# Optimization experiments

Hardware: AMD Instinct MI355X
Metric: run time of the kernel (lower is better)

The kernel has to match this reference:

```python
import jax, jax.numpy as jnp
import numpy as np

B, C, T, H = 2, 1024, 2048, 16
D = C // H  # head dim = 64
SCALE = 1.0 / np.sqrt(D)
NEG_INF = jnp.float32(-1e30)


def setup_inputs() -> dict:
    key = jax.random.key(0)
    ks = jax.random.split(key, 10)
    x = jax.random.normal(ks[0], (B, C, T), dtype=jnp.float32)
    mask = jax.random.randint(ks[1], (B, 1, T), 0, 2).astype(bool)
    mask = mask.at[:, :, 0].set(True)  # avoid all-masked rows -> NaN softmax
    w = 1.0 / np.sqrt(C)
    Wq = jax.random.normal(ks[2], (C, C), dtype=jnp.float32) * w
    bq = jax.random.normal(ks[3], (C,), dtype=jnp.float32) * 0.01
    Wk = jax.random.normal(ks[4], (C, C), dtype=jnp.float32) * w
    bk = jax.random.normal(ks[5], (C,), dtype=jnp.float32) * 0.01
    Wv = jax.random.normal(ks[6], (C, C), dtype=jnp.float32) * w
    bv = jax.random.normal(ks[7], (C,), dtype=jnp.float32) * 0.01
    Wp = jax.random.normal(ks[8], (C, C), dtype=jnp.float32) * w
    bp = jax.random.normal(ks[9], (C,), dtype=jnp.float32) * 0.01
    return {"x": x, "mask": mask, "Wq": Wq, "bq": bq, "Wk": Wk, "bk": bk,
            "Wv": Wv, "bv": bv, "Wp": Wp, "bp": bp}


def _proj(W, b, x):
    # Conv1d with kernel_size=1: per-timestep linear on [B, C, T]
    return jnp.einsum('oc,bct->bot', W, x) + b[:, None]


def _heads(y):
    # [B, C, T] -> [B, H, T, D]
    return y.reshape(B, H, D, T).transpose(0, 1, 3, 2)


def reference(x, mask, Wq, bq, Wk, bk, Wv, bv, Wp, bp):
    q = _heads(_proj(Wq, bq, x))  # [B,H,T,D]
    k = _heads(_proj(Wk, bk, x))
    v = _heads(_proj(Wv, bv, x))
    att = jnp.einsum('bhqd,bhkd->bhqk', q * SCALE, k)  # [B,H,T,T]
    att = jnp.where(mask[:, :, None, :], att, NEG_INF)  # mask keys
    att = jax.nn.softmax(att, axis=-1)
    vm = v * mask[:, :, :, None].astype(v.dtype)  # zero masked values
    out = jnp.einsum('bhqk,bhkd->bhqd', att, vm)  # [B,H,T,D]
    out = out.transpose(0, 1, 3, 2).reshape(B, C, T)
    out = _proj(Wp, bp, out) * mask.astype(x.dtype)  # [B,C,T]
    return (out, mask)
```

## Files before the change

### kernel.cpp

```cpp
#include <hip/hip_runtime.h>
#include <hip/hip_bf16.h>
#include <math.h>

#define BB 2
#define CC 1024
#define TT 2048
#define HH 16
#define DD 64

using short8   = __attribute__((ext_vector_type(8))) short;
using floatx4  = __attribute__((ext_vector_type(4))) float;
using floatx16 = __attribute__((ext_vector_type(16))) float;
typedef unsigned short ushort_t;

#define MFMA(a, b, c) __builtin_amdgcn_mfma_f32_16x16x32_bf16((a), (b), (c), 0, 0, 0)
#define MFMA32(a, b, c) __builtin_amdgcn_mfma_f32_32x32x16_bf16((a), (b), (c), 0, 0, 0)

#define QSC 0.18033688011112042f

#define PMAGIC   8404857.0f
#define PZERO_BF 0.97265625f

__device__ __forceinline__ ushort_t f2bf(float f) {
    unsigned int u = __float_as_uint(f);
    u += 0x7FFFu + ((u >> 16) & 1u);
    return (ushort_t)(u >> 16);
}
__device__ __forceinline__ float bf2f(ushort_t h) {
    return __uint_as_float(((unsigned int)h) << 16);
}
__device__ __forceinline__ ushort_t f2bf_t(float f) {
    return (ushort_t)(__float_as_uint(f) >> 16);
}
__device__ __forceinline__ unsigned int packtrunc(float a, float b) {
    return __builtin_amdgcn_perm(__float_as_uint(b), __float_as_uint(a),
                                 0x07060302u);
}
__device__ __forceinline__ unsigned int pack2bf_exp(float s0, float s1) {
    float f0 = fmaf(s0, 128.0f, PMAGIC);
    float f1 = fmaf(s1, 128.0f, PMAGIC);
    return __builtin_amdgcn_perm(__float_as_uint(f1), __float_as_uint(f0),
                                 0x05040100u);
}
__device__ __forceinline__ void load_lds16(const void* g, void* s) {
    __builtin_amdgcn_global_load_lds(
        (const __attribute__((address_space(1))) void*)g,
        (__attribute__((address_space(3))) void*)s, 16, 0, 0);
}

static constexpr size_t B0       = 65536;
static constexpr size_t XT_OFF   = B0;
static constexpr size_t WQKV_OFF = XT_OFF   + 8388608;
static constexpr size_t WP_OFF   = WQKV_OFF + 6291456;
static constexpr size_t Q_OFF    = WP_OFF   + 2097152;
static constexpr size_t K_OFF    = Q_OFF    + 8388608;
static constexpr size_t V_OFF    = K_OFF    + 8388608;
static constexpr size_t OP_OFF   = V_OFF    + 8388608;
static constexpr size_t ML_OFF   = OP_OFF   + 16777216;

__global__ __launch_bounds__(256) void prep_kernel(
    const float* __restrict__ x, const float* __restrict__ Wq,
    const float* __restrict__ Wk, const float* __restrict__ Wv,
    const float* __restrict__ Wp, const unsigned int* __restrict__ mraw,
    ushort_t* __restrict__ XT, ushort_t* __restrict__ WQKV,
    ushort_t* __restrict__ WP, float* __restrict__ maskf,
    int* __restrict__ nmcnt, float* __restrict__ out_tail) {
    __shared__ float tile[64][65];
    const int bid = blockIdx.x;
    const int tid = threadIdx.x;
    if (bid < 4096) {
        const int idx = bid * 256 + tid;
        if (idx < 786432) {
            int row = idx >> 8;
            int qc  = idx & 255;
            const float* src = row < 1024 ? Wq : (row < 2048 ? Wk : Wv);
            float4 v = *(const float4*)&src[(size_t)(row & 1023) * CC + qc * 4];
            ushort4 pk; pk.x = f2bf(v.x); pk.y = f2bf(v.y);
            pk.z = f2bf(v.z); pk.w = f2bf(v.w);
            *(ushort4*)&WQKV[(size_t)idx * 4] = pk;
        } else {
            int j = idx - 786432;
            float4 v = *(const float4*)&Wp[(size_t)j * 4];
            ushort4 pk; pk.x = f2bf(v.x); pk.y = f2bf(v.y);
            pk.z = f2bf(v.z); pk.w = f2bf(v.w);
            *(ushort4*)&WP[(size_t)j * 4] = pk;
        }
    } else if (bid < 5120) {
        const int xb = bid - 4096;
        const int t0 = (xb & 31) * 64, c0 = ((xb >> 5) & 15) * 64, b = xb >> 9;
        const int tc = tid & 15, tr = tid >> 4;
        #pragma unroll
        for (int p = 0; p < 4; p++) {
            int cl = tr + p * 16;
            float4 v = *(const float4*)&x[((size_t)b * CC + c0 + cl) * TT + t0 + tc * 4];
            tile[cl][tc * 4 + 0] = v.x; tile[cl][tc * 4 + 1] = v.y;
            tile[cl][tc * 4 + 2] = v.z; tile[cl][tc * 4 + 3] = v.w;
        }
        __syncthreads();
        #pragma unroll
        for (int p = 0; p < 4; p++) {
            int tl = tr + p * 16;
            ushort4 pk;
            pk.x = f2bf(tile[tc * 4 + 0][tl]);
            pk.y = f2bf(tile[tc * 4 + 1][tl]);
            pk.z = f2bf(tile[tc * 4 + 2][tl]);
            pk.w = f2bf(tile[tc * 4 + 3][tl]);
            *(ushort4*)&XT[((size_t)b * TT + t0 + tl) * CC + c0 + tc * 4] = pk;
        }
    } else {
        __shared__ int ev_bf16, ev_bool, cnt;
        const int mb = bid - 5120;
        if (tid == 0) { ev_bf16 = 0; ev_bool = 0; cnt = 0; }
        __syncthreads();
        for (int i = tid; i < 1024; i += 256) {
            unsigned int w = mraw[i];
            if ((w & 0xFFFFu) == 0x3F80u) atomicOr(&ev_bf16, 1);
            if ((w & 0xFFFFFF00u) != 0u && w != 0x3F800000u) atomicOr(&ev_bool, 1);
        }
        __syncthreads();
        const int mode = ev_bf16 ? 2 : (ev_bool ? 1 : 0);
        const int e = mb * 256 + tid;
        bool on;
        if (mode == 2)      on = ((const ushort_t*)mraw)[e] != 0;
        else if (mode == 1) on = ((const unsigned char*)mraw)[e] != 0;
        else                on = mraw[e] != 0;
        maskf[e]    = on ? 1.0f : 0.0f;
        out_tail[e] = on ? 1.0f : 0.0f;
        if (!on) atomicAdd(&cnt, 1);
        __syncthreads();
        if (tid == 0) nmcnt[mb] = cnt;
    }
}

__global__ __launch_bounds__(256) void gemm_qkv_kernel(
    const ushort_t* __restrict__ Wqkv, const float* __restrict__ bq,
    const float* __restrict__ bk, const float* __restrict__ bv,
    const ushort_t* __restrict__ XT, const float* __restrict__ maskf,
    ushort_t* __restrict__ Qo, ushort_t* __restrict__ Ko,
    ushort_t* __restrict__ Vo) {
    __shared__ ushort_t As[128][32];
    __shared__ ushort_t Bs[128][32];
    __shared__ float biasS[128];

    const int b = blockIdx.z;
    const int m0 = blockIdx.y * 128;
    const int n0 = blockIdx.x * 128;
    const int tid = threadIdx.x;
    const int lane = tid & 63;
    const int w = tid >> 6;
    const int wm = (w & 1) * 64, wn = (w >> 1) * 64;
    const int la = lane & 15, lg = lane >> 4;
    const int region = m0 >> 10;

    const float* bsrc = region == 0 ? (bq + m0)
                      : (region == 1 ? (bk + m0 - 1024) : (bv + m0 - 2048));
    if (tid < 128) biasS[tid] = bsrc[tid];

    float csc[4];
    #pragma unroll
    for (int nt = 0; nt < 4; nt++) {
        const int t = n0 + wn + nt * 16 + la;
        csc[nt] = (region == 0) ? QSC : maskf[b * TT + t];
    }

    floatx4 zero4 = {0.f, 0.f, 0.f, 0.f};
    floatx4 acc[4][4];
    #pragma unroll
    for (int mt = 0; mt < 4; mt++)
        #pragma unroll
        for (int nt = 0; nt < 4; nt++) acc[mt][nt] = zero4;

    const ushort_t* Abase = Wqkv + (size_t)m0 * CC;
    const ushort_t* Bbase = XT + ((size_t)b * TT + n0) * CC;
    const int rl = lane >> 2;
    const int cl = (lane & 3) * 8;

    for (int k0 = 0; k0 < CC; k0 += 32) {
        #pragma unroll
        for (int c = 0; c < 2; c++) {
            int row = w * 32 + c * 16;
            load_lds16(Abase + (size_t)(row + rl) * CC + k0 + cl, &As[row][0]);
            load_lds16(Bbase + (size_t)(row + rl) * CC + k0 + cl, &Bs[row][0]);
        }
        __syncthreads();
        short8 af[4], bf[4];
        #pragma unroll
        for (int mt = 0; mt < 4; mt++)
            af[mt] = *(const short8*)&As[wm + mt * 16 + la][lg * 8];
        #pragma unroll
        for (int nt = 0; nt < 4; nt++)
            bf[nt] = *(const short8*)&Bs[wn + nt * 16 + la][lg * 8];
        #pragma unroll
        for (int mt = 0; mt < 4; mt++)
            #pragma unroll
            for (int nt = 0; nt < 4; nt++)
                acc[mt][nt] = MFMA(af[mt], bf[nt], acc[mt][nt]);
        __syncthreads();
    }

    #pragma unroll
    for (int mt = 0; mt < 4; mt++) {
        const int lm = wm + mt * 16 + lg * 4;
        const int gm = m0 + lm;
        #pragma unroll
        for (int nt = 0; nt < 4; nt++) {
            const int t = n0 + wn + nt * 16 + la;
            const float sc = csc[nt];
            float v0 = (acc[mt][nt][0] + biasS[lm + 0]) * sc;
            float v1 = (acc[mt][nt][1] + biasS[lm + 1]) * sc;
            float v2 = (acc[mt][nt][2] + biasS[lm + 2]) * sc;
            float v3 = (acc[mt][nt][3] + biasS[lm + 3]) * sc;
            if (region < 2) {
                int mq = gm & 1023;
                int hh = mq >> 6, db = mq & 63;
                ushort_t* dst = (region == 0 ? Qo : Ko)
                              + (((size_t)b * HH + hh) * TT + t) * DD + db;
                uint2 pk;
                pk.x = packtrunc(v0, v1);
                pk.y = packtrunc(v2, v3);
                *(uint2*)dst = pk;
            } else {
                int c = gm & 1023;
                Vo[((size_t)b * CC + c + 0) * TT + t] = f2bf_t(v0);
                Vo[((size_t)b * CC + c + 1) * TT + t] = f2bf_t(v1);
                Vo[((size_t)b * CC + c + 2) * TT + t] = f2bf_t(v2);
                Vo[((size_t)b * CC + c + 3) * TT + t] = f2bf_t(v3);
            }
        }
    }
}

__global__ __launch_bounds__(256) void attn_kernel(
    const ushort_t* __restrict__ Qg, const ushort_t* __restrict__ Kg,
    const ushort_t* __restrict__ Vg, const int* __restrict__ nmcnt,
    ushort_t* __restrict__ Opart, float* __restrict__ lbuf) {
    __shared__ ushort_t Ks[2][64][72];
    __shared__ ushort_t Vs[2][64][72];

    const int sp = blockIdx.z & 1, b = blockIdx.z >> 1;
    const int hh = blockIdx.y, t0 = blockIdx.x * 128;
    const int j0base = sp * (TT / 2);
    const int tid  = threadIdx.x;
    const int lane = tid & 63;
    const int w    = tid >> 6;
    const int ln31 = lane & 31;
    const int h    = lane >> 5;
    const size_t qkbase = ((size_t)b * HH + hh) * TT * DD;
    const size_t vbase  = ((size_t)b * CC + hh * DD) * TT;

    const int tq = t0 + w * 32 + ln31;
    short8 qreg[4];
    {
        const ushort_t* qp = Qg + qkbase + (size_t)tq * DD + h * 8;
        #pragma unroll
        for (int kc = 0; kc < 4; kc++)
            qreg[kc] = *(const short8*)(qp + kc * 16);
    }

    const int srow = tid >> 2;
    const int scol = (tid & 3) * 16;
    const ushort_t* kbase = Kg + qkbase + (size_t)srow * DD + scol;
    const ushort_t* vbptr = Vg + vbase + (size_t)srow * TT + scol;

    int4 kpre0, kpre1, vpre0, vpre1;
    {
        const ushort_t* kp = kbase + (size_t)j0base * DD;
        const ushort_t* vp = vbptr + j0base;
        kpre0 = *(const int4*)(kp);  kpre1 = *(const int4*)(kp + 8);
        vpre0 = *(const int4*)(vp);  vpre1 = *(const int4*)(vp + 8);
    }

    floatx16 zero16 = {0.f,0.f,0.f,0.f,0.f,0.f,0.f,0.f,
                       0.f,0.f,0.f,0.f,0.f,0.f,0.f,0.f};
    floatx16 oacc[2];
    oacc[0] = zero16; oacc[1] = zero16;
    floatx16 lacc = zero16;
    short8 ones8;
    #pragma unroll
    for (int i = 0; i < 8; i++) ones8[i] = (short)0x3F80;

    for (int kt = 0; kt < 16; kt++) {
        const int p = kt & 1;
        *(int4*)&Ks[p][srow][scol]     = kpre0;
        *(int4*)&Ks[p][srow][scol + 8] = kpre1;
        *(int4*)&Vs[p][srow][scol]     = vpre0;
        *(int4*)&Vs[p][srow][scol + 8] = vpre1;
        __syncthreads();
        if (kt < 15) {
            const int j0n = j0base + (kt + 1) * 64;
            const ushort_t* kp = kbase + (size_t)j0n * DD;
            const ushort_t* vp = vbptr + j0n;
            kpre0 = *(const int4*)(kp);  kpre1 = *(const int4*)(kp + 8);
            vpre0 = *(const int4*)(vp);  vpre1 = *(const int4*)(vp + 8);
        }

        floatx16 sacc[2];
        sacc[0] = zero16; sacc[1] = zero16;
        #pragma unroll
        for (int kc = 0; kc < 4; kc++) {
            #pragma unroll
            for (int mt = 0; mt < 2; mt++) {
                short8 kf = *(const short8*)&Ks[p][mt * 32 + ln31][kc * 16 + h * 8];
                sacc[mt] = MFMA32(kf, qreg[kc], sacc[mt]);
            }
        }

        unsigned int pd[16];
        #pragma unroll
        for (int mt = 0; mt < 2; mt++)
            #pragma unroll
            for (int g = 0; g < 4; g++) {
                pd[mt * 8 + g * 2 + 0] =
                    pack2bf_exp(sacc[mt][g * 4 + 0], sacc[mt][g * 4 + 1]);
                pd[mt * 8 + g * 2 + 1] =
                    pack2bf_exp(sacc[mt][g * 4 + 2], sacc[mt][g * 4 + 3]);
            }

        #pragma unroll
        for (int kc = 0; kc < 4; kc++) {
            const int base = (kc >> 1) * 8 + (kc & 1) * 4;
            int a0 = pd[base], a1 = pd[base + 1], a2 = pd[base + 2], a3 = pd[base + 3];
            int x0 = __shfl_xor(h ? a0 : a2, 32, 64);
            int x1 = __shfl_xor(h ? a1 : a3, 32, 64);
            int4 fi;
            fi.x = h ? x0 : a0;
            fi.y = h ? x1 : a1;
            fi.z = h ? a2 : x0;
            fi.w = h ? a3 : x1;
            short8 pf = *(short8*)&fi;
            lacc = MFMA32(ones8, pf, lacc);
            #pragma unroll
            for (int dt = 0; dt < 2; dt++) {
                short8 vf = *(const short8*)&Vs[p][dt * 32 + ln31][kc * 16 + h * 8];
                oacc[dt] = MFMA32(vf, pf, oacc[dt]);
            }
        }
    }

    float lsum = lacc[0];
    {
        const int r4 = (b * 2 + sp) * 4;
        int nm = nmcnt[r4] + nmcnt[r4 + 1] + nmcnt[r4 + 2] + nmcnt[r4 + 3];
        lsum -= (float)nm * PZERO_BF;
    }

    const float inv = lsum > 0.0f ? 1.0f / lsum : 0.0f;
    ushort_t* OP = Opart + (size_t)sp * ((size_t)BB * TT * CC)
                 + ((size_t)b * TT + tq) * CC + hh * 64;
    #pragma unroll
    for (int mt = 0; mt < 2; mt++)
        #pragma unroll
        for (int g = 0; g < 4; g++) {
            int db = mt * 32 + g * 8 + h * 4;
            ushort4 pk;
            pk.x = f2bf(oacc[mt][g * 4 + 0] * inv);
            pk.y = f2bf(oacc[mt][g * 4 + 1] * inv);
            pk.z = f2bf(oacc[mt][g * 4 + 2] * inv);
            pk.w = f2bf(oacc[mt][g * 4 + 3] * inv);
            *(ushort4*)&OP[db] = pk;
        }
    if (h == 0)
        lbuf[(((size_t)sp * BB + b) * HH + hh) * TT + tq] = lsum;
}

__global__ __launch_bounds__(256) void combine_kernel(
    const ushort_t* __restrict__ Opart, const float* __restrict__ lbuf,
    ushort_t* __restrict__ OT) {
    const size_t idx = ((size_t)blockIdx.x * 256 + threadIdx.x) * 8;
    const int c0 = (int)(idx & (CC - 1));
    const int t  = (int)((idx >> 10) & (TT - 1));
    const int b  = (int)(idx >> 21);
    const int hh = c0 >> 6;
    const float l0 = lbuf[(((size_t)0 * BB + b) * HH + hh) * TT + t];
    const float l1 = lbuf[(((size_t)1 * BB + b) * HH + hh) * TT + t];
    const float sum = l0 + l1;
    const float ws = sum > 0.0f ? 1.0f / sum : 0.0f;
    const float w0 = l0 * ws, w1 = l1 * ws;
    const ushort_t* P0 = Opart + idx;
    const ushort_t* P1 = Opart + (size_t)BB * TT * CC + idx;
    ushort4 a0 = *(const ushort4*)(P0);
    ushort4 a1 = *(const ushort4*)(P0 + 4);
    ushort4 b0 = *(const ushort4*)(P1);
    ushort4 b1 = *(const ushort4*)(P1 + 4);
    ushort4 o0, o1;
    o0.x = f2bf(w0 * bf2f(a0.x) + w1 * bf2f(b0.x));
    o0.y = f2bf(w0 * bf2f(a0.y) + w1 * bf2f(b0.y));
    o0.z = f2bf(w0 * bf2f(a0.z) + w1 * bf2f(b0.z));
    o0.w = f2bf(w0 * bf2f(a0.w) + w1 * bf2f(b0.w));
    o1.x = f2bf(w0 * bf2f(a1.x) + w1 * bf2f(b1.x));
    o1.y = f2bf(w0 * bf2f(a1.y) + w1 * bf2f(b1.y));
    o1.z = f2bf(w0 * bf2f(a1.z) + w1 * bf2f(b1.z));
    o1.w = f2bf(w0 * bf2f(a1.w) + w1 * bf2f(b1.w));
    *(ushort4*)&OT[idx]     = o0;
    *(ushort4*)&OT[idx + 4] = o1;
}

__global__ __launch_bounds__(256) void gemm_out_kernel(
    const ushort_t* __restrict__ WP, const ushort_t* __restrict__ OT,
    const float* __restrict__ bp, const float* __restrict__ maskf,
    float* __restrict__ out) {
    __shared__ ushort_t As[64][32];
    __shared__ ushort_t Bs[128][32];
    __shared__ float biasS[64];

    const int b = blockIdx.z;
    const int m0 = blockIdx.y * 64;
    const int n0 = blockIdx.x * 128;
    const int tid = threadIdx.x;
    const int lane = tid & 63;
    const int w = tid >> 6;
    const int wm = (w & 1) * 32, wn = (w >> 1) * 64;
    const int la = lane & 15, lg = lane >> 4;

    if (tid < 64) biasS[tid] = bp[m0 + tid];

    floatx4 zero4 = {0.f, 0.f, 0.f, 0.f};
    floatx4 acc[2][4];
    #pragma unroll
    for (int mt = 0; mt < 2; mt++)
        #pragma unroll
        for (int nt = 0; nt < 4; nt++) acc[mt][nt] = zero4;

    const int rl = lane >> 2;
    const int cl = (lane & 3) * 8;
    const ushort_t* Bbase = OT + ((size_t)b * TT + n0) * CC;

    for (int k0 = 0; k0 < CC; k0 += 32) {
        {
            int row = w * 16;
            load_lds16(WP + (size_t)(m0 + row + rl) * CC + k0 + cl, &As[row][0]);
        }
        #pragma unroll
        for (int c = 0; c < 2; c++) {
            int row = w * 32 + c * 16;
            load_lds16(Bbase + (size_t)(row + rl) * CC + k0 + cl, &Bs[row][0]);
        }
        __syncthreads();
        short8 af[2], bf[4];
        #pragma unroll
        for (int mt = 0; mt < 2; mt++)
            af[mt] = *(const short8*)&As[wm + mt * 16 + la][lg * 8];
        #pragma unroll
        for (int nt = 0; nt < 4; nt++)
            bf[nt] = *(const short8*)&Bs[wn + nt * 16 + la][lg * 8];
        #pragma unroll
        for (int mt = 0; mt < 2; mt++)
            #pragma unroll
            for (int nt = 0; nt < 4; nt++)
                acc[mt][nt] = MFMA(af[mt], bf[nt], acc[mt][nt]);
        __syncthreads();
    }

    #pragma unroll
    for (int mt = 0; mt < 2; mt++) {
        const int lm = wm + mt * 16 + lg * 4;
        #pragma unroll
        for (int nt = 0; nt < 4; nt++) {
            const int t = n0 + wn + nt * 16 + la;
            const float mk = maskf[b * TT + t];
            #pragma unroll
            for (int r = 0; r < 4; r++)
                out[((size_t)b * CC + m0 + lm + r) * TT + t] =
                    (acc[mt][nt][r] + biasS[lm + r]) * mk;
        }
    }
}

extern "C" void kernel_launch(void* const* d_in, const int* in_sizes, int n_in,
                              void* d_out, int out_size, void* d_ws,
                              size_t ws_size, hipStream_t stream) {
    const float* x    = (const float*)d_in[0];
    const void*  mask = d_in[1];
    const float* Wq   = (const float*)d_in[2];
    const float* bq   = (const float*)d_in[3];
    const float* Wk   = (const float*)d_in[4];
    const float* bk   = (const float*)d_in[5];
    const float* Wv   = (const float*)d_in[6];
    const float* bv   = (const float*)d_in[7];
    const float* Wp   = (const float*)d_in[8];
    const float* bp   = (const float*)d_in[9];

    float* out  = (float*)d_out;
    float* wsf  = (float*)d_ws;
    int* nmcnt  = (int*)d_ws + 16;
    float* maskf = wsf + 1024;
    char* wsb = (char*)d_ws;
    ushort_t* XT    = (ushort_t*)(wsb + XT_OFF);
    ushort_t* WQKV  = (ushort_t*)(wsb + WQKV_OFF);
    ushort_t* WPb   = (ushort_t*)(wsb + WP_OFF);
    ushort_t* Qb    = (ushort_t*)(wsb + Q_OFF);
    ushort_t* Kb    = (ushort_t*)(wsb + K_OFF);
    ushort_t* Vb    = (ushort_t*)(wsb + V_OFF);
    ushort_t* Opart = (ushort_t*)(wsb + OP_OFF);
    float*    lbuf  = (float*)(wsb + ML_OFF);

    prep_kernel<<<5136, 256, 0, stream>>>(x, Wq, Wk, Wv, Wp,
                                          (const unsigned int*)mask, XT, WQKV,
                                          WPb, maskf, nmcnt,
                                          out + (size_t)BB * CC * TT);

    gemm_qkv_kernel<<<dim3(TT / 128, 3 * CC / 128, BB), 256, 0, stream>>>(
        WQKV, bq, bk, bv, XT, maskf, Qb, Kb, Vb);

    attn_kernel<<<dim3(TT / 128, HH, BB * 2), 256, 0, stream>>>(
        Qb, Kb, Vb, nmcnt, Opart, lbuf);

    combine_kernel<<<2048, 256, 0, stream>>>(Opart, lbuf, XT);

    gemm_out_kernel<<<dim3(TT / 128, CC / 64, BB), 256, 0, stream>>>(
        WPb, XT, bp, maskf, out);
}
```

Before: 202.3 us.

## Stream K/V tiles via direct global-to-LDS loads with XOR swizzle in attention

Replaces the register-staged K/V prefetch and padded LDS arrays with direct global-to-LDS async loads (load_lds16) into an XOR-swizzled, double-buffered LDS region. This removes the per-iteration register-to-LDS stores and one barrier. The cross-half lane exchange now uses permlane32_swap instead of two shuffles plus selects. It also adds s_setprio around the MFMA phases, a min-blocks launch bound of 4, and an unroll of 2, which may raise register pressure or cause spilling.

```diff
diff --git a/kernel.cpp b/kernel.cpp
--- a/kernel.cpp
+++ b/kernel.cpp
@@ -11,6 +11,7 @@
 using short8   = __attribute__((ext_vector_type(8))) short;
 using floatx4  = __attribute__((ext_vector_type(4))) float;
 using floatx16 = __attribute__((ext_vector_type(16))) float;
+using uint2v   = __attribute__((ext_vector_type(2))) unsigned int;
 typedef unsigned short ushort_t;
 
 #define MFMA(a, b, c) __builtin_amdgcn_mfma_f32_16x16x32_bf16((a), (b), (c), 0, 0, 0)
@@ -230,12 +231,11 @@
     }
 }
 
-__global__ __launch_bounds__(256) void attn_kernel(
+__global__ __launch_bounds__(256, 4) void attn_kernel(
     const ushort_t* __restrict__ Qg, const ushort_t* __restrict__ Kg,
     const ushort_t* __restrict__ Vg, const int* __restrict__ nmcnt,
     ushort_t* __restrict__ Opart, float* __restrict__ lbuf) {
-    __shared__ ushort_t Ks[2][64][72];
-    __shared__ ushort_t Vs[2][64][72];
+    __shared__ __align__(16) char ldsbuf[32768];
 
     const int sp = blockIdx.z & 1, b = blockIdx.z >> 1;
     const int hh = blockIdx.y, t0 = blockIdx.x * 128;
@@ -257,17 +257,19 @@
             qreg[kc] = *(const short8*)(qp + kc * 16);
     }
 
-    const int srow = tid >> 2;
-    const int scol = (tid & 3) * 16;
-    const ushort_t* kbase = Kg + qkbase + (size_t)srow * DD + scol;
-    const ushort_t* vbptr = Vg + vbase + (size_t)srow * TT + scol;
-
-    int4 kpre0, kpre1, vpre0, vpre1;
+    const int i3   = lane >> 3;
+    const int swzb = ((lane & 7) ^ i3) << 4;
+    const char* ks0 = (const char*)(Kg + qkbase + (size_t)(j0base + 16 * w + i3) * DD) + swzb;
+    const char* vs0 = (const char*)(Vg + vbase + (size_t)(16 * w + i3) * TT + j0base) + swzb;
+    char* kd = ldsbuf + 2 * w * 1024;
+    char* vd = ldsbuf + 16384 + 2 * w * 1024;
+
+    int ka[4];
     {
-        const ushort_t* kp = kbase + (size_t)j0base * DD;
-        const ushort_t* vp = vbptr + j0base;
-        kpre0 = *(const int4*)(kp);  kpre1 = *(const int4*)(kp + 8);
-        vpre0 = *(const int4*)(vp);  vpre1 = *(const int4*)(vp + 8);
+        const int kxor = (ln31 & 7) << 4;
+        #pragma unroll
+        for (int kc = 0; kc < 4; kc++)
+            ka[kc] = ln31 * 128 + ((kc * 32 + h * 16) ^ kxor);
     }
 
     floatx16 zero16 = {0.f,0.f,0.f,0.f,0.f,0.f,0.f,0.f,
@@ -279,31 +281,36 @@
     #pragma unroll
     for (int i = 0; i < 8; i++) ones8[i] = (short)0x3F80;
 
+    load_lds16(ks0,          kd);
+    load_lds16(ks0 + 1024,   kd + 1024);
+    load_lds16(vs0,          vd);
+    load_lds16(vs0 + 32768,  vd + 1024);
+    ks0 += 8192; vs0 += 128;
+    __syncthreads();
+
+    #pragma unroll 2
     for (int kt = 0; kt < 16; kt++) {
-        const int p = kt & 1;
-        *(int4*)&Ks[p][srow][scol]     = kpre0;
-        *(int4*)&Ks[p][srow][scol + 8] = kpre1;
-        *(int4*)&Vs[p][srow][scol]     = vpre0;
-        *(int4*)&Vs[p][srow][scol + 8] = vpre1;
-        __syncthreads();
+        const int pp = (kt & 1) * 8192;
+        const int pn = 8192 - pp;
         if (kt < 15) {
-            const int j0n = j0base + (kt + 1) * 64;
-            const ushort_t* kp = kbase + (size_t)j0n * DD;
-            const ushort_t* vp = vbptr + j0n;
-            kpre0 = *(const int4*)(kp);  kpre1 = *(const int4*)(kp + 8);
-            vpre0 = *(const int4*)(vp);  vpre1 = *(const int4*)(vp + 8);
+            load_lds16(ks0,         kd + pn);
+            load_lds16(ks0 + 1024,  kd + pn + 1024);
+            load_lds16(vs0,         vd + pn);
+            load_lds16(vs0 + 32768, vd + pn + 1024);
+            ks0 += 8192; vs0 += 128;
         }
 
         floatx16 sacc[2];
         sacc[0] = zero16; sacc[1] = zero16;
+        __builtin_amdgcn_s_setprio(1);
         #pragma unroll
         for (int kc = 0; kc < 4; kc++) {
-            #pragma unroll
-            for (int mt = 0; mt < 2; mt++) {
-                short8 kf = *(const short8*)&Ks[p][mt * 32 + ln31][kc * 16 + h * 8];
-                sacc[mt] = MFMA32(kf, qreg[kc], sacc[mt]);
-            }
-        }
+            short8 kf0 = *(const short8*)(ldsbuf + ka[kc] + pp);
+            short8 kf1 = *(const short8*)(ldsbuf + ka[kc] + pp + 4096);
+            sacc[0] = MFMA32(kf0, qreg[kc], sacc[0]);
+            sacc[1] = MFMA32(kf1, qreg[kc], sacc[1]);
+        }
+        __builtin_amdgcn_s_setprio(0);
 
         unsigned int pd[16];
         #pragma unroll
@@ -316,25 +323,29 @@
                     pack2bf_exp(sacc[mt][g * 4 + 2], sacc[mt][g * 4 + 3]);
             }
 
+        __builtin_amdgcn_s_setprio(1);
         #pragma unroll
         for (int kc = 0; kc < 4; kc++) {
             const int base = (kc >> 1) * 8 + (kc & 1) * 4;
-            int a0 = pd[base], a1 = pd[base + 1], a2 = pd[base + 2], a3 = pd[base + 3];
-            int x0 = __shfl_xor(h ? a0 : a2, 32, 64);
-            int x1 = __shfl_xor(h ? a1 : a3, 32, 64);
+            uint2v r02 = __builtin_amdgcn_permlane32_swap(
+                pd[base + 0], pd[base + 2], false, false);
+            uint2v r13 = __builtin_amdgcn_permlane32_swap(
+                pd[base + 1], pd[base + 3], false, false);
             int4 fi;
-            fi.x = h ? x0 : a0;
-            fi.y = h ? x1 : a1;
-            fi.z = h ? a2 : x0;
-            fi.w = h ? a3 : x1;
+            fi.x = (int)r02[0];
+            fi.y = (int)r13[0];
+            fi.z = (int)r02[1];
+            fi.w = (int)r13[1];
             short8 pf = *(short8*)&fi;
             lacc = MFMA32(ones8, pf, lacc);
-            #pragma unroll
-            for (int dt = 0; dt < 2; dt++) {
-                short8 vf = *(const short8*)&Vs[p][dt * 32 + ln31][kc * 16 + h * 8];
-                oacc[dt] = MFMA32(vf, pf, oacc[dt]);
-            }
-        }
+            short8 vf0 = *(const short8*)(ldsbuf + ka[kc] + pp + 16384);
+            short8 vf1 = *(const short8*)(ldsbuf + ka[kc] + pp + 16384 + 4096);
+            oacc[0] = MFMA32(vf0, pf, oacc[0]);
+            oacc[1] = MFMA32(vf1, pf, oacc[1]);
+        }
+        __builtin_amdgcn_s_setprio(0);
+
+        if (kt < 15) __syncthreads();
     }
 
     float lsum = lacc[0];
```

Result: faster. 192.6 us (-4.8%).
